# Kernel tuning notes

Measured on AMD Instinct MI355X. Metric: run time of the kernel, lower is better.

## Reference

```python
import jax, jax.numpy as jnp
import numpy as np

D = 4096  # domain size of every variable X, Y, Z, W


def setup_inputs() -> dict:
    key = jax.random.key(0)
    ks = jax.random.split(key, 7)
    theta0 = jax.random.normal(ks[0], (D, D), dtype=jnp.float32)  # clique (X, Y)
    theta1 = jax.random.normal(ks[1], (D, D), dtype=jnp.float32)  # clique (Y, Z)
    theta2 = jax.random.normal(ks[2], (D, D), dtype=jnp.float32)  # clique (Z, W)
    ops = {f"op{i}": jax.random.randint(ks[3 + i], (2, D), 0, D, dtype=jnp.int32)
           for i in range(4)}
    return {"theta0": theta0, "theta1": theta1, "theta2": theta2, **ops}


def _remap(proc, op, dom):
    # torch: zeros(dom).index_add_(0, op[1], proc[op[0]])
    return jnp.zeros((dom,), proc.dtype).at[op[1]].add(proc[op[0]])


def reference(theta0, theta1, theta2, op0, op1, op2, op3):
    dom = theta0.shape[0]
    # m0: clique0 -> clique1 (forward): sum over X (dim 0), remap Y, broadcast over Z
    m0 = _remap(jnp.sum(theta0, axis=0), op0, dom)
    theta1 = theta1 + m0[:, None]          # reshape_dims [True, False]
    # m1: clique1 -> clique2 (forward): sum over Y (dim 0), remap Z
    m1 = _remap(jnp.sum(theta1, axis=0), op1, dom)
    theta2 = theta2 + m1[:, None]
    # m2: clique2 -> clique1 (backward): sum over W (dim 1), subtract stored fwd msg m1
    m2 = _remap(jnp.sum(theta2, axis=1) - m1, op2, dom)
    theta1 = theta1 + m2[None, :]          # reshape_dims [False, True]
    # m3: clique1 -> clique0 (backward): sum over Z (dim 1), subtract stored fwd msg m0
    m3 = _remap(jnp.sum(theta1, axis=1) - m0, op3, dom)
    theta0 = theta0 + m3[None, :]
    return (theta0, theta1, theta2)
```

## Files before the change

kernel.cpp:

```cpp
#include <hip/hip_runtime.h>

#define D 4096

typedef float fx4 __attribute__((ext_vector_type(4)));

#define CS0 0
#define CS1 D
#define RS1 (2 * D)
#define RS2 (3 * D)
#define MSG (4 * D)

__global__ void __launch_bounds__(256) reduce_all_kernel(
        const float* __restrict__ t0, const float* __restrict__ t1,
        const float* __restrict__ t2, float* __restrict__ ws) {
    int b = blockIdx.x;
    if (b < 512) {
        const float* A = (b < 256) ? t0 : t1;
        float* out = ws + ((b < 256) ? CS0 : CS1);
        int lb = b & 255;
        int c4 = (lb & 3) * 256 + threadIdx.x;
        int r0 = (lb >> 2) * 64;
        const fx4* A4 = (const fx4*)A;
        fx4 s = (fx4){0.f, 0.f, 0.f, 0.f};
        #pragma unroll 8
        for (int r = 0; r < 64; ++r)
            s += A4[(size_t)(r0 + r) * (D / 4) + c4];
        atomicAdd(&out[c4 * 4 + 0], s.x);
        atomicAdd(&out[c4 * 4 + 1], s.y);
        atomicAdd(&out[c4 * 4 + 2], s.z);
        atomicAdd(&out[c4 * 4 + 3], s.w);
    } else {
        int lb = (b - 512) & 1023;
        const float* A = (b < 1536) ? t1 : t2;
        float* out = ws + ((b < 1536) ? RS1 : RS2);
        int wid = threadIdx.x >> 6, lane = threadIdx.x & 63;
        int row = lb * 4 + wid;
        const fx4* R = (const fx4*)(A + (size_t)row * D);
        float s = 0.f;
        #pragma unroll
        for (int j = 0; j < 16; ++j) {
            fx4 v = R[lane + 64 * j];
            s += (v.x + v.y) + (v.z + v.w);
        }
        #pragma unroll
        for (int o = 32; o > 0; o >>= 1) s += __shfl_down(s, o);
        if (lane == 0) out[row] = s;
    }
}


__device__ __forceinline__ float block_sum_1024(float v, float* red) {
    #pragma unroll
    for (int o = 32; o > 0; o >>= 1) v += __shfl_down(v, o);
    int lane = threadIdx.x & 63, wid = threadIdx.x >> 6;
    if (lane == 0) red[wid] = v;
    __syncthreads();
    if (threadIdx.x == 0) {
        float t = 0.f;
        #pragma unroll
        for (int w = 0; w < 16; ++w) t += red[w];
        red[0] = t;
    }
    __syncthreads();
    float r = red[0];
    __syncthreads();
    return r;
}

__global__ void __launch_bounds__(1024) messages_kernel(
        const float* __restrict__ ws,
        const int* __restrict__ op0, const int* __restrict__ op1,
        const int* __restrict__ op2, const int* __restrict__ op3,
        float* __restrict__ ws_w) {
    __shared__ float m0[D], m1[D], m2[D], m3[D];
    __shared__ float red[16];
    int tid = threadIdx.x;

    int s0[4], d0[4], s1[4], d1[4], s2[4], d2[4], s3[4], d3[4];
    #pragma unroll
    for (int k = 0; k < 4; ++k) {
        int i = tid + k * 1024;
        s0[k] = op0[i]; d0[k] = op0[D + i];
        s1[k] = op1[i]; d1[k] = op1[D + i];
        s2[k] = op2[i]; d2[k] = op2[D + i];
        s3[k] = op3[i]; d3[k] = op3[D + i];
    }
    float g0[4], g1[4], g2[4], g3[4];
    #pragma unroll
    for (int k = 0; k < 4; ++k) {
        g0[k] = ws[CS0 + s0[k]];
        g1[k] = ws[CS1 + s1[k]];
        g2[k] = ws[RS2 + s2[k]];
        g3[k] = ws[RS1 + s3[k]];
    }

    #pragma unroll
    for (int k = 0; k < 4; ++k) {
        int i = tid + k * 1024;
        m0[i] = 0.f; m1[i] = 0.f; m2[i] = 0.f; m3[i] = 0.f;
    }
    __syncthreads();

    #pragma unroll
    for (int k = 0; k < 4; ++k) atomicAdd(&m0[d0[k]], g0[k]);
    __syncthreads();

    float p = 0.f;
    #pragma unroll
    for (int k = 0; k < 4; ++k) p += m0[tid + k * 1024];
    float S0 = block_sum_1024(p, red);

    #pragma unroll
    for (int k = 0; k < 4; ++k) atomicAdd(&m1[d1[k]], g1[k] + S0);
    __syncthreads();

    #pragma unroll
    for (int k = 0; k < 4; ++k)
        atomicAdd(&m2[d2[k]], g2[k] + 4095.0f * m1[s2[k]]);
    __syncthreads();

    p = 0.f;
    #pragma unroll
    for (int k = 0; k < 4; ++k) p += m2[tid + k * 1024];
    float S2 = block_sum_1024(p, red);

    #pragma unroll
    for (int k = 0; k < 4; ++k)
        atomicAdd(&m3[d3[k]], g3[k] + 4095.0f * m0[s3[k]] + S2);
    __syncthreads();

    #pragma unroll
    for (int k = 0; k < 4; ++k) {
        int i = tid + k * 1024;
        ws_w[MSG + 0 * D + i] = m0[i];
        ws_w[MSG + 1 * D + i] = m1[i];
        ws_w[MSG + 2 * D + i] = m2[i];
        ws_w[MSG + 3 * D + i] = m3[i];
    }
}


template <int MODE>
__global__ void __launch_bounds__(256) apply_one_kernel(
        const float* __restrict__ t, const float* __restrict__ msgs,
        float* __restrict__ outm) {
    int row = blockIdx.x;
    size_t base = (size_t)row * D;
    const fx4* src = (const fx4*)(t + base);
    fx4* dst = (fx4*)(outm + base);

    if (MODE == 0) {
        const fx4* c4 = (const fx4*)(msgs + 3 * D);
        for (int i = threadIdx.x; i < D / 4; i += 256) {
            fx4 r = src[i] + c4[i];
            __builtin_nontemporal_store(r, &dst[i]);
        }
    } else if (MODE == 1) {
        const fx4* c4 = (const fx4*)(msgs + 2 * D);
        float rr = msgs[0 * D + row];
        for (int i = threadIdx.x; i < D / 4; i += 256) {
            fx4 r = src[i] + c4[i] + rr;
            __builtin_nontemporal_store(r, &dst[i]);
        }
    } else {
        float rr = msgs[1 * D + row];
        for (int i = threadIdx.x; i < D / 4; i += 256) {
            fx4 r = src[i] + rr;
            __builtin_nontemporal_store(r, &dst[i]);
        }
    }
}

extern "C" void kernel_launch(void* const* d_in, const int* in_sizes, int n_in,
                              void* d_out, int out_size, void* d_ws, size_t ws_size,
                              hipStream_t stream) {
    const float* t0 = (const float*)d_in[0];
    const float* t1 = (const float*)d_in[1];
    const float* t2 = (const float*)d_in[2];
    const int* op0 = (const int*)d_in[3];
    const int* op1 = (const int*)d_in[4];
    const int* op2 = (const int*)d_in[5];
    const int* op3 = (const int*)d_in[6];
    float* out = (float*)d_out;
    float* ws = (float*)d_ws;

    hipMemsetAsync(ws, 0, 2 * D * sizeof(float), stream);

    reduce_all_kernel<<<2560, 256, 0, stream>>>(t0, t1, t2, ws);
    messages_kernel<<<1, 1024, 0, stream>>>(ws, op0, op1, op2, op3, ws);
    apply_one_kernel<2><<<D, 256, 0, stream>>>(t2, ws + MSG, out + 2 * (size_t)D * D);
    apply_one_kernel<1><<<D, 256, 0, stream>>>(t1, ws + MSG, out + 1 * (size_t)D * D);
    apply_one_kernel<0><<<D, 256, 0, stream>>>(t0, ws + MSG, out + 0 * (size_t)D * D);
}
```

Baseline: 149.7 us.

## Fuse row sums of theta1/theta2 into apply passes, split message kernel into stages

Drops the separate row-sum reads of theta1 and theta2 by computing them inside the apply kernels that already stream those rows, and splits the single message kernel into three staged kernels placed between the apply passes. This cuts one full read of two 64MB matrices. In exchange it adds two more serialized single-block kernel launches and breaks the pipeline into a longer dependent chain.

Result: faster. 135.0 us (median of 2 runs) (-9.9%).

```diff
diff --git a/kernel.cpp b/kernel.cpp
--- a/kernel.cpp
+++ b/kernel.cpp
@@ -8,44 +8,30 @@
 #define CS1 D
 #define RS1 (2 * D)
 #define RS2 (3 * D)
-#define MSG (4 * D)
-
-__global__ void __launch_bounds__(256) reduce_all_kernel(
+#define M0O (4 * D)
+#define M1O (5 * D)
+#define M2O (6 * D)
+#define M3O (7 * D)
+#define S2S (8 * D)
+
+__global__ void __launch_bounds__(256) colsum_kernel(
         const float* __restrict__ t0, const float* __restrict__ t1,
-        const float* __restrict__ t2, float* __restrict__ ws) {
+        float* __restrict__ ws) {
     int b = blockIdx.x;
-    if (b < 512) {
-        const float* A = (b < 256) ? t0 : t1;
-        float* out = ws + ((b < 256) ? CS0 : CS1);
-        int lb = b & 255;
-        int c4 = (lb & 3) * 256 + threadIdx.x;
-        int r0 = (lb >> 2) * 64;
-        const fx4* A4 = (const fx4*)A;
-        fx4 s = (fx4){0.f, 0.f, 0.f, 0.f};
-        #pragma unroll 8
-        for (int r = 0; r < 64; ++r)
-            s += A4[(size_t)(r0 + r) * (D / 4) + c4];
-        atomicAdd(&out[c4 * 4 + 0], s.x);
-        atomicAdd(&out[c4 * 4 + 1], s.y);
-        atomicAdd(&out[c4 * 4 + 2], s.z);
-        atomicAdd(&out[c4 * 4 + 3], s.w);
-    } else {
-        int lb = (b - 512) & 1023;
-        const float* A = (b < 1536) ? t1 : t2;
-        float* out = ws + ((b < 1536) ? RS1 : RS2);
-        int wid = threadIdx.x >> 6, lane = threadIdx.x & 63;
-        int row = lb * 4 + wid;
-        const fx4* R = (const fx4*)(A + (size_t)row * D);
-        float s = 0.f;
-        #pragma unroll
-        for (int j = 0; j < 16; ++j) {
-            fx4 v = R[lane + 64 * j];
-            s += (v.x + v.y) + (v.z + v.w);
-        }
-        #pragma unroll
-        for (int o = 32; o > 0; o >>= 1) s += __shfl_down(s, o);
-        if (lane == 0) out[row] = s;
-    }
+    const float* A = (b < 256) ? t0 : t1;
+    float* out = ws + ((b < 256) ? CS0 : CS1);
+    int lb = b & 255;
+    int c4 = (lb & 3) * 256 + threadIdx.x;
+    int r0 = (lb >> 2) * 64;
+    const fx4* A4 = (const fx4*)A;
+    fx4 s = (fx4){0.f, 0.f, 0.f, 0.f};
+    #pragma unroll 8
+    for (int r = 0; r < 64; ++r)
+        s += A4[(size_t)(r0 + r) * (D / 4) + c4];
+    atomicAdd(&out[c4 * 4 + 0], s.x);
+    atomicAdd(&out[c4 * 4 + 1], s.y);
+    atomicAdd(&out[c4 * 4 + 2], s.z);
+    atomicAdd(&out[c4 * 4 + 3], s.w);
 }
 
 
@@ -67,107 +53,184 @@
     return r;
 }
 
-__global__ void __launch_bounds__(1024) messages_kernel(
-        const float* __restrict__ ws,
-        const int* __restrict__ op0, const int* __restrict__ op1,
-        const int* __restrict__ op2, const int* __restrict__ op3,
-        float* __restrict__ ws_w) {
-    __shared__ float m0[D], m1[D], m2[D], m3[D];
+__global__ void __launch_bounds__(1024) msgsA_kernel(
+        float* __restrict__ ws, const int* __restrict__ op0,
+        const int* __restrict__ op1) {
+    __shared__ float m0[D], m1[D];
     __shared__ float red[16];
     int tid = threadIdx.x;
 
-    int s0[4], d0[4], s1[4], d1[4], s2[4], d2[4], s3[4], d3[4];
+    int s0[4], d0[4], s1[4], d1[4];
     #pragma unroll
     for (int k = 0; k < 4; ++k) {
         int i = tid + k * 1024;
         s0[k] = op0[i]; d0[k] = op0[D + i];
         s1[k] = op1[i]; d1[k] = op1[D + i];
-        s2[k] = op2[i]; d2[k] = op2[D + i];
-        s3[k] = op3[i]; d3[k] = op3[D + i];
-    }
-    float g0[4], g1[4], g2[4], g3[4];
+    }
+    float g0[4], g1[4];
     #pragma unroll
     for (int k = 0; k < 4; ++k) {
         g0[k] = ws[CS0 + s0[k]];
         g1[k] = ws[CS1 + s1[k]];
-        g2[k] = ws[RS2 + s2[k]];
-        g3[k] = ws[RS1 + s3[k]];
-    }
-
-    #pragma unroll
-    for (int k = 0; k < 4; ++k) {
-        int i = tid + k * 1024;
-        m0[i] = 0.f; m1[i] = 0.f; m2[i] = 0.f; m3[i] = 0.f;
-    }
-    __syncthreads();
-
+    }
+    #pragma unroll
+    for (int k = 0; k < 4; ++k) {
+        int i = tid + k * 1024;
+        m0[i] = 0.f; m1[i] = 0.f;
+    }
+    __syncthreads();
     #pragma unroll
     for (int k = 0; k < 4; ++k) atomicAdd(&m0[d0[k]], g0[k]);
     __syncthreads();
-
     float p = 0.f;
     #pragma unroll
     for (int k = 0; k < 4; ++k) p += m0[tid + k * 1024];
     float S0 = block_sum_1024(p, red);
-
     #pragma unroll
     for (int k = 0; k < 4; ++k) atomicAdd(&m1[d1[k]], g1[k] + S0);
     __syncthreads();
-
-    #pragma unroll
-    for (int k = 0; k < 4; ++k)
-        atomicAdd(&m2[d2[k]], g2[k] + 4095.0f * m1[s2[k]]);
-    __syncthreads();
-
-    p = 0.f;
+    #pragma unroll
+    for (int k = 0; k < 4; ++k) {
+        int i = tid + k * 1024;
+        ws[M0O + i] = m0[i];
+        ws[M1O + i] = m1[i];
+    }
+}
+
+__global__ void __launch_bounds__(1024) msgsB_kernel(
+        float* __restrict__ ws, const int* __restrict__ op2) {
+    __shared__ float m2[D];
+    __shared__ float red[16];
+    int tid = threadIdx.x;
+
+    int s2[4], d2[4];
+    #pragma unroll
+    for (int k = 0; k < 4; ++k) {
+        int i = tid + k * 1024;
+        s2[k] = op2[i]; d2[k] = op2[D + i];
+    }
+    float g2[4];
+    #pragma unroll
+    for (int k = 0; k < 4; ++k)
+        g2[k] = ws[RS2 + s2[k]] + 4095.0f * ws[M1O + s2[k]];
+    #pragma unroll
+    for (int k = 0; k < 4; ++k) m2[tid + k * 1024] = 0.f;
+    __syncthreads();
+    #pragma unroll
+    for (int k = 0; k < 4; ++k) atomicAdd(&m2[d2[k]], g2[k]);
+    __syncthreads();
+    float p = 0.f;
     #pragma unroll
     for (int k = 0; k < 4; ++k) p += m2[tid + k * 1024];
     float S2 = block_sum_1024(p, red);
-
-    #pragma unroll
-    for (int k = 0; k < 4; ++k)
-        atomicAdd(&m3[d3[k]], g3[k] + 4095.0f * m0[s3[k]] + S2);
-    __syncthreads();
-
-    #pragma unroll
-    for (int k = 0; k < 4; ++k) {
-        int i = tid + k * 1024;
-        ws_w[MSG + 0 * D + i] = m0[i];
-        ws_w[MSG + 1 * D + i] = m1[i];
-        ws_w[MSG + 2 * D + i] = m2[i];
-        ws_w[MSG + 3 * D + i] = m3[i];
-    }
-}
-
-
-template <int MODE>
-__global__ void __launch_bounds__(256) apply_one_kernel(
-        const float* __restrict__ t, const float* __restrict__ msgs,
-        float* __restrict__ outm) {
+    #pragma unroll
+    for (int k = 0; k < 4; ++k) {
+        int i = tid + k * 1024;
+        ws[M2O + i] = m2[i];
+    }
+    if (tid == 0) ws[S2S] = S2;
+}
+
+__global__ void __launch_bounds__(1024) msgsC_kernel(
+        float* __restrict__ ws, const int* __restrict__ op3) {
+    __shared__ float m3[D];
+    int tid = threadIdx.x;
+
+    int s3[4], d3[4];
+    #pragma unroll
+    for (int k = 0; k < 4; ++k) {
+        int i = tid + k * 1024;
+        s3[k] = op3[i]; d3[k] = op3[D + i];
+    }
+    float S2 = ws[S2S];
+    float g3[4];
+    #pragma unroll
+    for (int k = 0; k < 4; ++k)
+        g3[k] = ws[RS1 + s3[k]] + 4095.0f * ws[M0O + s3[k]] + S2;
+    #pragma unroll
+    for (int k = 0; k < 4; ++k) m3[tid + k * 1024] = 0.f;
+    __syncthreads();
+    #pragma unroll
+    for (int k = 0; k < 4; ++k) atomicAdd(&m3[d3[k]], g3[k]);
+    __syncthreads();
+    #pragma unroll
+    for (int k = 0; k < 4; ++k) {
+        int i = tid + k * 1024;
+        ws[M3O + i] = m3[i];
+    }
+}
+
+
+__device__ __forceinline__ void row_reduce_store(float s, float* dst) {
+    __shared__ float red[4];
+    #pragma unroll
+    for (int o = 32; o > 0; o >>= 1) s += __shfl_down(s, o);
+    int lane = threadIdx.x & 63, wid = threadIdx.x >> 6;
+    if (lane == 0) red[wid] = s;
+    __syncthreads();
+    if (threadIdx.x == 0) *dst = (red[0] + red[1]) + (red[2] + red[3]);
+}
+
+__global__ void __launch_bounds__(256) applyT2_kernel(
+        const float* __restrict__ t2, float* __restrict__ ws,
+        float* __restrict__ out2) {
     int row = blockIdx.x;
     size_t base = (size_t)row * D;
-    const fx4* src = (const fx4*)(t + base);
-    fx4* dst = (fx4*)(outm + base);
-
-    if (MODE == 0) {
-        const fx4* c4 = (const fx4*)(msgs + 3 * D);
-        for (int i = threadIdx.x; i < D / 4; i += 256) {
-            fx4 r = src[i] + c4[i];
-            __builtin_nontemporal_store(r, &dst[i]);
-        }
-    } else if (MODE == 1) {
-        const fx4* c4 = (const fx4*)(msgs + 2 * D);
-        float rr = msgs[0 * D + row];
-        for (int i = threadIdx.x; i < D / 4; i += 256) {
-            fx4 r = src[i] + c4[i] + rr;
-            __builtin_nontemporal_store(r, &dst[i]);
-        }
-    } else {
-        float rr = msgs[1 * D + row];
-        for (int i = threadIdx.x; i < D / 4; i += 256) {
-            fx4 r = src[i] + rr;
-            __builtin_nontemporal_store(r, &dst[i]);
-        }
+    const fx4* src = (const fx4*)(t2 + base);
+    fx4* dst = (fx4*)(out2 + base);
+    float rr = ws[M1O + row];
+
+    fx4 v[4];
+    float s = 0.f;
+    #pragma unroll
+    for (int k = 0; k < 4; ++k) {
+        v[k] = src[threadIdx.x + 256 * k];
+        s += (v[k].x + v[k].y) + (v[k].z + v[k].w);
+    }
+    #pragma unroll
+    for (int k = 0; k < 4; ++k)
+        __builtin_nontemporal_store(v[k] + rr, &dst[threadIdx.x + 256 * k]);
+    row_reduce_store(s, ws + RS2 + row);
+}
+
+__global__ void __launch_bounds__(256) applyT1_kernel(
+        const float* __restrict__ t1, float* __restrict__ ws,
+        float* __restrict__ out1) {
+    int row = blockIdx.x;
+    size_t base = (size_t)row * D;
+    const fx4* src = (const fx4*)(t1 + base);
+    const fx4* c4 = (const fx4*)(ws + M2O);
+    fx4* dst = (fx4*)(out1 + base);
+    float rr = ws[M0O + row];
+
+    fx4 v[4], c[4];
+    float s = 0.f;
+    #pragma unroll
+    for (int k = 0; k < 4; ++k) {
+        v[k] = src[threadIdx.x + 256 * k];
+        c[k] = c4[threadIdx.x + 256 * k];
+        s += (v[k].x + v[k].y) + (v[k].z + v[k].w);
+    }
+    #pragma unroll
+    for (int k = 0; k < 4; ++k)
+        __builtin_nontemporal_store(v[k] + c[k] + rr,
+                                    &dst[threadIdx.x + 256 * k]);
+    row_reduce_store(s, ws + RS1 + row);
+}
+
+__global__ void __launch_bounds__(256) applyT0_kernel(
+        const float* __restrict__ t0, const float* __restrict__ ws,
+        float* __restrict__ out0) {
+    int row = blockIdx.x;
+    size_t base = (size_t)row * D;
+    const fx4* src = (const fx4*)(t0 + base);
+    const fx4* c4 = (const fx4*)(ws + M3O);
+    fx4* dst = (fx4*)(out0 + base);
+
+    #pragma unroll
+    for (int k = 0; k < 4; ++k) {
+        fx4 r = src[threadIdx.x + 256 * k] + c4[threadIdx.x + 256 * k];
+        __builtin_nontemporal_store(r, &dst[threadIdx.x + 256 * k]);
     }
 }
 
@@ -186,9 +249,11 @@
 
     hipMemsetAsync(ws, 0, 2 * D * sizeof(float), stream);
 
-    reduce_all_kernel<<<2560, 256, 0, stream>>>(t0, t1, t2, ws);
-    messages_kernel<<<1, 1024, 0, stream>>>(ws, op0, op1, op2, op3, ws);
-    apply_one_kernel<2><<<D, 256, 0, stream>>>(t2, ws + MSG, out + 2 * (size_t)D * D);
-    apply_one_kernel<1><<<D, 256, 0, stream>>>(t1, ws + MSG, out + 1 * (size_t)D * D);
-    apply_one_kernel<0><<<D, 256, 0, stream>>>(t0, ws + MSG, out + 0 * (size_t)D * D);
-}
+    colsum_kernel<<<512, 256, 0, stream>>>(t0, t1, ws);
+    msgsA_kernel<<<1, 1024, 0, stream>>>(ws, op0, op1);
+    applyT2_kernel<<<D, 256, 0, stream>>>(t2, ws, out + 2 * (size_t)D * D);
+    msgsB_kernel<<<1, 1024, 0, stream>>>(ws, op2);
+    applyT1_kernel<<<D, 256, 0, stream>>>(t1, ws, out + 1 * (size_t)D * D);
+    msgsC_kernel<<<1, 1024, 0, stream>>>(ws, op3);
+    applyT0_kernel<<<D, 256, 0, stream>>>(t0, ws, out + 0 * (size_t)D * D);
+}
```
